# Kernel optimization log

Hardware: AMD Instinct MI355X
Metric: run time of the kernel (lower is better)

The kernel has to match this reference:

```python
import jax, jax.numpy as jnp
import numpy as np

B, DIN, DOUT, K = 2048, 2048, 2048, 16

def setup_inputs() -> dict:
    key = jax.random.key(0)
    k1, k2, k3 = jax.random.split(key, 3)
    # init scale from reset_parameters: s = 3**0.5 / ((din+dout)/2 * k)**0.25
    d = (DIN + DOUT) / 2.0
    s = 3.0 ** 0.5 / (d * K) ** 0.25
    x = jax.random.normal(k1, (B, DIN), dtype=jnp.float32)
    w1 = jax.random.uniform(k2, (DIN, DOUT, K), minval=-s, maxval=s, dtype=jnp.float32)
    w2 = jax.random.uniform(k3, (DIN, DOUT, K), minval=-s, maxval=s, dtype=jnp.float32)
    b1 = jnp.zeros((DOUT, K), dtype=jnp.float32)
    b2 = jnp.zeros((DOUT,), dtype=jnp.float32)
    return {"x": x, "w1": w1, "b1": b1, "w2": w2, "b2": b2}

def reference(x, w1, b1, w2, b2):
    # g: [b, o, k] gating mixture, relu-activated
    g = jax.nn.relu(jnp.einsum('bi,iok->bok', x, w1) + b1)
    # three-way contraction over i and k -> [b, o]
    out = jnp.einsum('bi,iok,bok->bo', x, w2, g) + b2
    return out
```

## Files before the change

kernel.cpp:

```cpp
#include <hip/hip_runtime.h>
#include <hip/hip_bf16.h>


typedef __bf16 bf16;
typedef bf16 bf16x8 __attribute__((ext_vector_type(8)));
typedef bf16 bf16x4 __attribute__((ext_vector_type(4)));
typedef float f32x4 __attribute__((ext_vector_type(4)));

typedef __attribute__((address_space(1))) const void gco_void;
typedef __attribute__((address_space(3))) void lds_void;

#define DIN_   2048
#define DOUT_  2048
#define NP_    32768

__device__ __forceinline__ bf16x8 cvt8(f32x4 a, f32x4 b) {
    bf16x8 v;
    v[0] = (bf16)a[0]; v[1] = (bf16)a[1]; v[2] = (bf16)a[2]; v[3] = (bf16)a[3];
    v[4] = (bf16)b[0]; v[5] = (bf16)b[1]; v[6] = (bf16)b[2]; v[7] = (bf16)b[3];
    return v;
}

__global__ __launch_bounds__(256)
void xcvt(const float* __restrict__ x, bf16* __restrict__ xb) {
    const size_t i = ((size_t)blockIdx.x * 256 + threadIdx.x) * 8;
    f32x4 a = *(const f32x4*)(x + i);
    f32x4 b = *(const f32x4*)(x + i + 4);
    *(bf16x8*)(xb + i) = cvt8(a, b);
}

__global__ __launch_bounds__(256)
void wtrans(const float* __restrict__ w1, const float* __restrict__ w2,
            bf16* __restrict__ w1t, bf16* __restrict__ w2t) {
    __shared__ float s[64][65];
    const int t  = threadIdx.x;
    const int lr = t >> 4;
    const int lq = t & 15;
    const int n0 = blockIdx.x * 64;
    const int i0 = blockIdx.y * 64;
    const float* src = blockIdx.z ? w2 : w1;
    bf16*        dst = blockIdx.z ? w2t : w1t;
#pragma unroll
    for (int r = 0; r < 4; ++r) {
        const int il = lr + 16 * r;
        f32x4 v = *(const f32x4*)(src + (size_t)(i0 + il) * NP_ + n0 + lq * 4);
        s[il][lq * 4 + 0] = v[0]; s[il][lq * 4 + 1] = v[1];
        s[il][lq * 4 + 2] = v[2]; s[il][lq * 4 + 3] = v[3];
    }
    __syncthreads();
#pragma unroll
    for (int r = 0; r < 4; ++r) {
        const int nl = lr + 16 * r;
        bf16x4 o;
        o[0] = (bf16)s[lq * 4 + 0][nl]; o[1] = (bf16)s[lq * 4 + 1][nl];
        o[2] = (bf16)s[lq * 4 + 2][nl]; o[3] = (bf16)s[lq * 4 + 3][nl];
        *(bf16x4*)(dst + (size_t)(n0 + nl) * DIN_ + i0 + lq * 4) = o;
    }
}

#define SYNC8() do { asm volatile("s_waitcnt vmcnt(8)" ::: "memory"); \
    __builtin_amdgcn_s_barrier(); __builtin_amdgcn_sched_barrier(0); } while (0)
#define SYNC4() do { asm volatile("s_waitcnt vmcnt(4)" ::: "memory"); \
    __builtin_amdgcn_s_barrier(); __builtin_amdgcn_sched_barrier(0); } while (0)
#define SYNC0() do { asm volatile("s_waitcnt vmcnt(0)" ::: "memory"); \
    __builtin_amdgcn_s_barrier(); __builtin_amdgcn_sched_barrier(0); } while (0)

__global__ __launch_bounds__(512, 2)
void mix2_gemmr(const bf16* __restrict__ xb, const bf16* __restrict__ w1t,
                const bf16* __restrict__ w2t, const float* __restrict__ b1,
                const float* __restrict__ b2, float* __restrict__ out)
{
    __shared__ alignas(16) char lds[131072];

    const int tid  = threadIdx.x;
    const int lane = tid & 63;
    const int wid  = tid >> 6;
    const int wm   = wid >> 2;
    const int wn   = wid & 3;
    const int lk   = lane & 15;
    const int lg   = lane >> 4;

    const int nwg = gridDim.x;
    const int bid = (blockIdx.x & 7) * (nwg >> 3) + (blockIdx.x >> 3);
    const int mt  = bid & 7;
    const int nt  = bid >> 3;

    const int srow = tid >> 2;
    const int sswz = ((tid & 3) ^ ((srow >> 1) & 3)) * 8;
    const bf16* gA  = xb  + (size_t)(mt * 256 + srow) * DIN_ + sswz;
    const bf16* gB1 = w1t + (size_t)(nt * 128 + srow) * DIN_ + sswz;
    const bf16* gB2 = w2t + (size_t)(nt * 128 + srow) * DIN_ + sswz;

    const int kswz = (lg ^ ((lk >> 1) & 3)) * 16;
    int aoff[8], boff[2];
#pragma unroll
    for (int fm = 0; fm < 8; ++fm) aoff[fm] = (wm * 128 + fm * 16 + lk) * 64 + kswz;
#pragma unroll
    for (int fn = 0; fn < 2; ++fn) boff[fn] = (wn * 32 + fn * 16 + lk) * 64 + kswz;

    f32x4 acc1[8][2], acc2[8][2];
#pragma unroll
    for (int i = 0; i < 8; ++i)
#pragma unroll
        for (int j = 0; j < 2; ++j) {
            acc1[i][j] = (f32x4){0.f, 0.f, 0.f, 0.f};
            acc2[i][j] = (f32x4){0.f, 0.f, 0.f, 0.f};
        }

    const int ldw = wid * 1024;
    auto STG = [&](int h) {
        char* r = lds + (h & 3) * 32768;
        const int koff = h * 32;
        __builtin_amdgcn_global_load_lds((gco_void*)(gA  + koff),             (lds_void*)(r +         ldw), 16, 0, 0);
        __builtin_amdgcn_global_load_lds((gco_void*)(gA + 128 * DIN_ + koff), (lds_void*)(r +  8192 + ldw), 16, 0, 0);
        __builtin_amdgcn_global_load_lds((gco_void*)(gB1 + koff),             (lds_void*)(r + 16384 + ldw), 16, 0, 0);
        __builtin_amdgcn_global_load_lds((gco_void*)(gB2 + koff),             (lds_void*)(r + 24576 + ldw), 16, 0, 0);
    };

    auto PHASE = [&](int h) {
        const char* r = lds + (h & 3) * 32768;
        bf16x8 a[8], u[2], v[2];
#pragma unroll
        for (int fn = 0; fn < 2; ++fn) {
            u[fn] = *(const bf16x8*)(r + 16384 + boff[fn]);
            v[fn] = *(const bf16x8*)(r + 24576 + boff[fn]);
        }
#pragma unroll
        for (int fm = 0; fm < 8; ++fm) a[fm] = *(const bf16x8*)(r + aoff[fm]);
        __builtin_amdgcn_s_setprio(1);
#pragma unroll
        for (int fm = 0; fm < 8; ++fm)
#pragma unroll
            for (int fn = 0; fn < 2; ++fn) {
                acc1[fm][fn] = __builtin_amdgcn_mfma_f32_16x16x32_bf16(a[fm], u[fn], acc1[fm][fn], 0, 0, 0);
                acc2[fm][fn] = __builtin_amdgcn_mfma_f32_16x16x32_bf16(a[fm], v[fn], acc2[fm][fn], 0, 0, 0);
            }
        __builtin_amdgcn_s_setprio(0);
    };

    STG(0); STG(1); STG(2);

#pragma unroll 1
    for (int t = 0; t < 15; ++t) {
        const int h0 = t * 4;
#pragma unroll
        for (int q = 0; q < 4; ++q) {
            SYNC8();
            STG(h0 + q + 3);
            PHASE(h0 + q);
        }
    }
    SYNC8(); STG(63); PHASE(60);
    SYNC8();          PHASE(61);
    SYNC4();          PHASE(62);
    SYNC0();          PHASE(63);

    const int obase = nt * 8 + wn * 2;
#pragma unroll
    for (int fn = 0; fn < 2; ++fn) {
        const int o = obase + fn;
        const float bb1 = b1[(size_t)o * 16 + lk];
        const float bb2 = b2[o];
#pragma unroll
        for (int fm = 0; fm < 8; ++fm) {
#pragma unroll
            for (int j = 0; j < 4; ++j) {
                float g = fmaxf(acc1[fm][fn][j] + bb1, 0.f);
                float p = g * acc2[fm][fn][j];
                p += __shfl_xor(p, 1);
                p += __shfl_xor(p, 2);
                p += __shfl_xor(p, 4);
                p += __shfl_xor(p, 8);
                if (lk == 0) {
                    const int brow = mt * 256 + wm * 128 + fm * 16 + lg * 4 + j;
                    out[(size_t)brow * DOUT_ + o] = p + bb2;
                }
            }
        }
    }
}

__global__ __launch_bounds__(512)
void mix2_fused_direct(const float* __restrict__ x, const float* __restrict__ w1,
                       const float* __restrict__ b1, const float* __restrict__ w2,
                       const float* __restrict__ b2, float* __restrict__ out)
{
    __shared__ alignas(16) char lds[2 * 49152];

    const int tid  = threadIdx.x;
    const int lane = tid & 63;
    const int wid  = tid >> 6;
    const int wm   = wid >> 2;
    const int wn   = wid & 3;

    const int nwg = gridDim.x;
    const int bid = (blockIdx.x & 7) * (nwg >> 3) + (blockIdx.x >> 3);
    const int mt  = bid & 15;
    const int nt  = bid >> 4;

    const int lk  = lane & 15;
    const int lg  = lane >> 4;
    const int swz = (lane & 7) << 4;

    const int a_row  = tid >> 3;
    const int a_col8 = tid & 7;
    const int b_ib = ((tid >> 5) & 15) << 2;
    const int b_nb = (tid & 31) << 2;

    const float* pa  = x  + (size_t)(mt * 128 + a_row) * DIN_ + a_col8 * 8;
    const float* pb1 = w1 + (size_t)b_ib * NP_ + (size_t)nt * 128 + b_nb;
    const float* pb2 = w2 + (size_t)b_ib * NP_ + (size_t)nt * 128 + b_nb;

    const int aswz   = (a_col8 * 16) ^ ((a_row & 7) << 4);
    const int aoffw0 = a_row * 128 + aswz;
    const int aoffw1 = (a_row + 64) * 128 + aswz;

    int aoff[4], boff1[2], boff2[2];
#pragma unroll
    for (int fm = 0; fm < 4; ++fm) aoff[fm] = (wm * 64 + fm * 16 + lk) * 128;
#pragma unroll
    for (int fn = 0; fn < 2; ++fn) {
        const int n = wn * 32 + fn * 16 + lk;
        boff1[fn] = 16384 + n * 128;
        boff2[fn] = 32768 + n * 128;
    }
    const int kp0 = (lg * 16) ^ swz;
    const int kp1 = (64 + lg * 16) ^ swz;

    f32x4 acc1[4][2], acc2[4][2];
#pragma unroll
    for (int i = 0; i < 4; ++i)
#pragma unroll
        for (int j = 0; j < 2; ++j) {
            acc1[i][j] = (f32x4){0.f, 0.f, 0.f, 0.f};
            acc2[i][j] = (f32x4){0.f, 0.f, 0.f, 0.f};
        }

    f32x4 rA[4], rB1[4], rB2[4];

    auto LOAD = [&](int kt) {
        const float* a0 = pa + kt * 64;
        rA[0] = *(const f32x4*)(a0);
        rA[1] = *(const f32x4*)(a0 + 4);
        rA[2] = *(const f32x4*)(a0 + (size_t)64 * DIN_);
        rA[3] = *(const f32x4*)(a0 + (size_t)64 * DIN_ + 4);
        const float* q1 = pb1 + (size_t)kt * 64 * NP_;
        const float* q2 = pb2 + (size_t)kt * 64 * NP_;
#pragma unroll
        for (int j = 0; j < 4; ++j) {
            rB1[j] = *(const f32x4*)(q1 + (size_t)j * NP_);
            rB2[j] = *(const f32x4*)(q2 + (size_t)j * NP_);
        }
    };

    auto STORE = [&](char* s) {
        *(bf16x8*)(s + aoffw0) = cvt8(rA[0], rA[1]);
        *(bf16x8*)(s + aoffw1) = cvt8(rA[2], rA[3]);
        char* s1 = s + 16384;
        char* s2 = s + 32768;
#pragma unroll
        for (int c = 0; c < 4; ++c) {
            const int n   = b_nb + c;
            const int off = n * 128 + ((b_ib * 2) ^ ((n & 7) << 4));
            bf16x4 v1, v2;
            v1[0] = (bf16)rB1[0][c]; v1[1] = (bf16)rB1[1][c];
            v1[2] = (bf16)rB1[2][c]; v1[3] = (bf16)rB1[3][c];
            v2[0] = (bf16)rB2[0][c]; v2[1] = (bf16)rB2[1][c];
            v2[2] = (bf16)rB2[2][c]; v2[3] = (bf16)rB2[3][c];
            *(bf16x4*)(s1 + off) = v1;
            *(bf16x4*)(s2 + off) = v2;
        }
    };

    auto COMPUTE = [&](const char* s) {
#pragma unroll
        for (int kb = 0; kb < 2; ++kb) {
            const int kp = kb ? kp1 : kp0;
            bf16x8 a[4], u[2], v[2];
#pragma unroll
            for (int fm = 0; fm < 4; ++fm) a[fm] = *(const bf16x8*)(s + aoff[fm] + kp);
#pragma unroll
            for (int fn = 0; fn < 2; ++fn) u[fn] = *(const bf16x8*)(s + boff1[fn] + kp);
#pragma unroll
            for (int fn = 0; fn < 2; ++fn) v[fn] = *(const bf16x8*)(s + boff2[fn] + kp);
#pragma unroll
            for (int fm = 0; fm < 4; ++fm)
#pragma unroll
                for (int fn = 0; fn < 2; ++fn) {
                    acc1[fm][fn] = __builtin_amdgcn_mfma_f32_16x16x32_bf16(a[fm], u[fn], acc1[fm][fn], 0, 0, 0);
                    acc2[fm][fn] = __builtin_amdgcn_mfma_f32_16x16x32_bf16(a[fm], v[fn], acc2[fm][fn], 0, 0, 0);
                }
        }
    };

    char* buf0 = lds;
    char* buf1 = lds + 49152;

    LOAD(0);
    STORE(buf0);
    __syncthreads();

    for (int kt = 0; kt < 32; ++kt) {
        if (kt + 1 < 32) LOAD(kt + 1);
        COMPUTE((kt & 1) ? buf1 : buf0);
        if (kt + 1 < 32) {
            STORE((kt & 1) ? buf0 : buf1);
            __syncthreads();
        }
    }

    const int obase = nt * 8 + wn * 2;
#pragma unroll
    for (int fn = 0; fn < 2; ++fn) {
        const int o = obase + fn;
        const float bb1 = b1[(size_t)o * 16 + lk];
        const float bb2 = b2[o];
#pragma unroll
        for (int fm = 0; fm < 4; ++fm) {
#pragma unroll
            for (int j = 0; j < 4; ++j) {
                float g = fmaxf(acc1[fm][fn][j] + bb1, 0.f);
                float p = g * acc2[fm][fn][j];
                p += __shfl_xor(p, 1);
                p += __shfl_xor(p, 2);
                p += __shfl_xor(p, 4);
                p += __shfl_xor(p, 8);
                if (lk == 0) {
                    const int brow = mt * 128 + wm * 64 + fm * 16 + lg * 4 + j;
                    out[(size_t)brow * DOUT_ + o] = p + bb2;
                }
            }
        }
    }
}

extern "C" void kernel_launch(void* const* d_in, const int* in_sizes, int n_in,
                              void* d_out, int out_size, void* d_ws, size_t ws_size,
                              hipStream_t stream) {
    (void)in_sizes; (void)n_in; (void)out_size;
    const float* x  = (const float*)d_in[0];
    const float* w1 = (const float*)d_in[1];
    const float* b1 = (const float*)d_in[2];
    const float* w2 = (const float*)d_in[3];
    const float* b2 = (const float*)d_in[4];
    float* out = (float*)d_out;

    const size_t XB   = (size_t)DIN_ * DIN_ * 2;
    const size_t WT   = (size_t)NP_ * DIN_ * 2;
    const size_t NEED = XB + 2 * WT;

    if (ws_size >= NEED) {
        bf16* xb  = (bf16*)d_ws;
        bf16* w1t = (bf16*)((char*)d_ws + XB);
        bf16* w2t = (bf16*)((char*)d_ws + XB + WT);
        hipLaunchKernelGGL(xcvt,   dim3(2048),       dim3(256), 0, stream, x, xb);
        hipLaunchKernelGGL(wtrans, dim3(512, 32, 2), dim3(256), 0, stream, w1, w2, w1t, w2t);
        hipLaunchKernelGGL(mix2_gemmr, dim3(2048),   dim3(512), 0, stream, xb, w1t, w2t, b1, b2, out);
    } else {
        hipLaunchKernelGGL(mix2_fused_direct, dim3(4096), dim3(512), 0, stream, x, w1, b1, w2, b2, out);
    }
}
```

Baseline: 683.1 us.

## Split each K-step into two ping-pong halves interleaving loads and MFMA

Restructures the main GEMM loop so each K-step runs as two halves. Each half reads part of the A fragments from LDS, issues half of the next stage's global-to-LDS loads, then runs a block of MFMAs between barriers. This is the 8-wave ping-pong pattern, meant to overlap LDS reads and global loads with matrix work across the two co-resident workgroups. It adds more barriers per step, and the vmcnt waits in the tail must still match the pipeline depth for correctness.

```diff
diff --git a/kernel.cpp b/kernel.cpp
--- a/kernel.cpp
+++ b/kernel.cpp
@@ -58,17 +58,10 @@
     }
 }
 
-#define SYNC8() do { asm volatile("s_waitcnt vmcnt(8)" ::: "memory"); \
-    __builtin_amdgcn_s_barrier(); __builtin_amdgcn_sched_barrier(0); } while (0)
-#define SYNC4() do { asm volatile("s_waitcnt vmcnt(4)" ::: "memory"); \
-    __builtin_amdgcn_s_barrier(); __builtin_amdgcn_sched_barrier(0); } while (0)
-#define SYNC0() do { asm volatile("s_waitcnt vmcnt(0)" ::: "memory"); \
-    __builtin_amdgcn_s_barrier(); __builtin_amdgcn_sched_barrier(0); } while (0)
-
 __global__ __launch_bounds__(512, 2)
-void mix2_gemmr(const bf16* __restrict__ xb, const bf16* __restrict__ w1t,
-                const bf16* __restrict__ w2t, const float* __restrict__ b1,
-                const float* __restrict__ b2, float* __restrict__ out)
+void mix2_gemm8p(const bf16* __restrict__ xb, const bf16* __restrict__ w1t,
+                 const bf16* __restrict__ w2t, const float* __restrict__ b1,
+                 const float* __restrict__ b2, float* __restrict__ out)
 {
     __shared__ alignas(16) char lds[131072];
 
@@ -108,52 +101,78 @@
         }
 
     const int ldw = wid * 1024;
-    auto STG = [&](int h) {
+    auto STG_A = [&](int h) {
         char* r = lds + (h & 3) * 32768;
         const int koff = h * 32;
-        __builtin_amdgcn_global_load_lds((gco_void*)(gA  + koff),             (lds_void*)(r +         ldw), 16, 0, 0);
-        __builtin_amdgcn_global_load_lds((gco_void*)(gA + 128 * DIN_ + koff), (lds_void*)(r +  8192 + ldw), 16, 0, 0);
-        __builtin_amdgcn_global_load_lds((gco_void*)(gB1 + koff),             (lds_void*)(r + 16384 + ldw), 16, 0, 0);
-        __builtin_amdgcn_global_load_lds((gco_void*)(gB2 + koff),             (lds_void*)(r + 24576 + ldw), 16, 0, 0);
-    };
-
-    auto PHASE = [&](int h) {
-        const char* r = lds + (h & 3) * 32768;
-        bf16x8 a[8], u[2], v[2];
-#pragma unroll
-        for (int fn = 0; fn < 2; ++fn) {
-            u[fn] = *(const bf16x8*)(r + 16384 + boff[fn]);
-            v[fn] = *(const bf16x8*)(r + 24576 + boff[fn]);
-        }
-#pragma unroll
-        for (int fm = 0; fm < 8; ++fm) a[fm] = *(const bf16x8*)(r + aoff[fm]);
-        __builtin_amdgcn_s_setprio(1);
-#pragma unroll
-        for (int fm = 0; fm < 8; ++fm)
-#pragma unroll
-            for (int fn = 0; fn < 2; ++fn) {
-                acc1[fm][fn] = __builtin_amdgcn_mfma_f32_16x16x32_bf16(a[fm], u[fn], acc1[fm][fn], 0, 0, 0);
-                acc2[fm][fn] = __builtin_amdgcn_mfma_f32_16x16x32_bf16(a[fm], v[fn], acc2[fm][fn], 0, 0, 0);
-            }
-        __builtin_amdgcn_s_setprio(0);
-    };
-
-    STG(0); STG(1); STG(2);
+        __builtin_amdgcn_global_load_lds((gco_void*)(gA  + koff),             (lds_void*)(r +        ldw), 16, 0, 0);
+        __builtin_amdgcn_global_load_lds((gco_void*)(gA + 128 * DIN_ + koff), (lds_void*)(r + 8192 + ldw), 16, 0, 0);
+    };
+    auto STG_B = [&](int h) {
+        char* r = lds + (h & 3) * 32768;
+        const int koff = h * 32;
+        __builtin_amdgcn_global_load_lds((gco_void*)(gB1 + koff), (lds_void*)(r + 16384 + ldw), 16, 0, 0);
+        __builtin_amdgcn_global_load_lds((gco_void*)(gB2 + koff), (lds_void*)(r + 24576 + ldw), 16, 0, 0);
+    };
+
+#define HALF(h, DO_STG, W) do {                                              \
+    const char* r_ = lds + (((h) & 3) * 32768);                              \
+    bf16x8 u[2], v[2], a0[4], a1[4];                                         \
+                                                      \
+    _Pragma("unroll") for (int fn_ = 0; fn_ < 2; ++fn_) {                    \
+        u[fn_] = *(const bf16x8*)(r_ + 16384 + boff[fn_]);                   \
+        v[fn_] = *(const bf16x8*)(r_ + 24576 + boff[fn_]);                   \
+    }                                                                        \
+    _Pragma("unroll") for (int j_ = 0; j_ < 4; ++j_)                         \
+        a0[j_] = *(const bf16x8*)(r_ + aoff[j_]);                            \
+    if (DO_STG) STG_A((h) + 3);                                              \
+    __builtin_amdgcn_s_barrier();                                            \
+    asm volatile("s_waitcnt lgkmcnt(0)" ::: "memory");                       \
+    __builtin_amdgcn_sched_barrier(0);                                       \
+    __builtin_amdgcn_s_setprio(1);                                           \
+    _Pragma("unroll") for (int j_ = 0; j_ < 4; ++j_)                         \
+        _Pragma("unroll") for (int fn_ = 0; fn_ < 2; ++fn_) {                \
+            acc1[j_][fn_] = __builtin_amdgcn_mfma_f32_16x16x32_bf16(a0[j_], u[fn_], acc1[j_][fn_], 0, 0, 0); \
+            acc2[j_][fn_] = __builtin_amdgcn_mfma_f32_16x16x32_bf16(a0[j_], v[fn_], acc2[j_][fn_], 0, 0, 0); \
+        }                                                                    \
+    __builtin_amdgcn_s_setprio(0);                                           \
+    __builtin_amdgcn_s_barrier();                                            \
+                                                      \
+    _Pragma("unroll") for (int j_ = 0; j_ < 4; ++j_)                         \
+        a1[j_] = *(const bf16x8*)(r_ + aoff[4 + j_]);                        \
+    if (DO_STG) STG_B((h) + 3);                                              \
+    __builtin_amdgcn_s_barrier();                                            \
+    asm volatile("s_waitcnt lgkmcnt(0)" ::: "memory");                       \
+    __builtin_amdgcn_sched_barrier(0);                                       \
+    __builtin_amdgcn_s_setprio(1);                                           \
+    _Pragma("unroll") for (int j_ = 0; j_ < 4; ++j_)                         \
+        _Pragma("unroll") for (int fn_ = 0; fn_ < 2; ++fn_) {                \
+            acc1[4 + j_][fn_] = __builtin_amdgcn_mfma_f32_16x16x32_bf16(a1[j_], u[fn_], acc1[4 + j_][fn_], 0, 0, 0); \
+            acc2[4 + j_][fn_] = __builtin_amdgcn_mfma_f32_16x16x32_bf16(a1[j_], v[fn_], acc2[4 + j_][fn_], 0, 0, 0); \
+        }                                                                    \
+    __builtin_amdgcn_s_setprio(0);                                           \
+    asm volatile("s_waitcnt vmcnt(" #W ")" ::: "memory");                    \
+    __builtin_amdgcn_s_barrier();                                            \
+} while (0)
+
+    STG_A(0); STG_B(0); STG_A(1); STG_B(1); STG_A(2); STG_B(2);
+    asm volatile("s_waitcnt vmcnt(8)" ::: "memory");
+    __builtin_amdgcn_s_barrier();
+    __builtin_amdgcn_sched_barrier(0);
 
 #pragma unroll 1
     for (int t = 0; t < 15; ++t) {
         const int h0 = t * 4;
-#pragma unroll
-        for (int q = 0; q < 4; ++q) {
-            SYNC8();
-            STG(h0 + q + 3);
-            PHASE(h0 + q);
-        }
-    }
-    SYNC8(); STG(63); PHASE(60);
-    SYNC8();          PHASE(61);
-    SYNC4();          PHASE(62);
-    SYNC0();          PHASE(63);
+        HALF(h0 + 0, true, 8);
+        HALF(h0 + 1, true, 8);
+        HALF(h0 + 2, true, 8);
+        HALF(h0 + 3, true, 8);
+    }
+    HALF(60, true, 8);
+    HALF(61, false, 4);
+    HALF(62, false, 0);
+    HALF(63, false, 0);
+
+#undef HALF
 
     const int obase = nt * 8 + wn * 2;
 #pragma unroll
@@ -355,7 +374,7 @@
         bf16* w2t = (bf16*)((char*)d_ws + XB + WT);
         hipLaunchKernelGGL(xcvt,   dim3(2048),       dim3(256), 0, stream, x, xb);
         hipLaunchKernelGGL(wtrans, dim3(512, 32, 2), dim3(256), 0, stream, w1, w2, w1t, w2t);
-        hipLaunchKernelGGL(mix2_gemmr, dim3(2048),   dim3(512), 0, stream, xb, w1t, w2t, b1, b2, out);
+        hipLaunchKernelGGL(mix2_gemm8p, dim3(2048),  dim3(512), 0, stream, xb, w1t, w2t, b1, b2, out);
     } else {
         hipLaunchKernelGGL(mix2_fused_direct, dim3(4096), dim3(512), 0, stream, x, w1, b1, w2, b2, out);
     }
```

New measurement: 680.1 us. No clear change (-0.4%).

## Split GEMM workgroup into 16 waves with halved per-wave M tile

Applied to the files above, without the earlier changes.

Grows the main GEMM workgroup from 512 to 1024 threads (16 waves) on the same 256x128 output tile. Each wave now covers 64 rows instead of 128, which halves its accumulators and A-fragment registers. Global-to-LDS staging is redistributed so each thread issues two loads per stage instead of four, and the vmcnt waits are adjusted to match. The aim is more waves per CU for latency hiding, since the launch bound goes from (512,2) to (1024,1). The cost is the same LDS use per block with more waves contending at each barrier, and every B fragment is now re-read from LDS by twice as many waves.

```diff
diff --git a/kernel.cpp b/kernel.cpp
--- a/kernel.cpp
+++ b/kernel.cpp
@@ -58,17 +58,10 @@
     }
 }
 
-#define SYNC8() do { asm volatile("s_waitcnt vmcnt(8)" ::: "memory"); \
-    __builtin_amdgcn_s_barrier(); __builtin_amdgcn_sched_barrier(0); } while (0)
-#define SYNC4() do { asm volatile("s_waitcnt vmcnt(4)" ::: "memory"); \
-    __builtin_amdgcn_s_barrier(); __builtin_amdgcn_sched_barrier(0); } while (0)
-#define SYNC0() do { asm volatile("s_waitcnt vmcnt(0)" ::: "memory"); \
-    __builtin_amdgcn_s_barrier(); __builtin_amdgcn_sched_barrier(0); } while (0)
-
-__global__ __launch_bounds__(512, 2)
-void mix2_gemmr(const bf16* __restrict__ xb, const bf16* __restrict__ w1t,
-                const bf16* __restrict__ w2t, const float* __restrict__ b1,
-                const float* __restrict__ b2, float* __restrict__ out)
+__global__ __launch_bounds__(1024, 1)
+void mix2_gemm16w(const bf16* __restrict__ xb, const bf16* __restrict__ w1t,
+                  const bf16* __restrict__ w2t, const float* __restrict__ b1,
+                  const float* __restrict__ b2, float* __restrict__ out)
 {
     __shared__ alignas(16) char lds[131072];
 
@@ -85,51 +78,52 @@
     const int mt  = bid & 7;
     const int nt  = bid >> 3;
 
-    const int srow = tid >> 2;
-    const int sswz = ((tid & 3) ^ ((srow >> 1) & 3)) * 8;
-    const bf16* gA  = xb  + (size_t)(mt * 256 + srow) * DIN_ + sswz;
-    const bf16* gB1 = w1t + (size_t)(nt * 128 + srow) * DIN_ + sswz;
-    const bf16* gB2 = w2t + (size_t)(nt * 128 + srow) * DIN_ + sswz;
+    const int arow = tid >> 2;
+    const int aswz = ((tid & 3) ^ ((arow >> 1) & 3)) * 8;
+    const int tb   = tid & 511;
+    const int brow = tb >> 2;
+    const int bswz = ((tb & 3) ^ ((brow >> 1) & 3)) * 8;
+    const bf16* gA = xb + (size_t)(mt * 256 + arow) * DIN_ + aswz;
+    const bf16* gB = (tid < 512 ? w1t : w2t) + (size_t)(nt * 128 + brow) * DIN_ + bswz;
+    const int adst = arow * 64 + (tid & 3) * 16;
+    const int bdst = 16384 + (tid >= 512 ? 8192 : 0) + tb * 16;
 
     const int kswz = (lg ^ ((lk >> 1) & 3)) * 16;
-    int aoff[8], boff[2];
-#pragma unroll
-    for (int fm = 0; fm < 8; ++fm) aoff[fm] = (wm * 128 + fm * 16 + lk) * 64 + kswz;
-#pragma unroll
-    for (int fn = 0; fn < 2; ++fn) boff[fn] = (wn * 32 + fn * 16 + lk) * 64 + kswz;
-
-    f32x4 acc1[8][2], acc2[8][2];
-#pragma unroll
-    for (int i = 0; i < 8; ++i)
+    int aoff[4], boff[2];
+#pragma unroll
+    for (int fm = 0; fm < 4; ++fm) aoff[fm] = (wm * 64 + fm * 16 + lk) * 64 + kswz;
+#pragma unroll
+    for (int fn = 0; fn < 2; ++fn) boff[fn] = 16384 + (wn * 32 + fn * 16 + lk) * 64 + kswz;
+
+    f32x4 acc1[4][2], acc2[4][2];
+#pragma unroll
+    for (int i = 0; i < 4; ++i)
 #pragma unroll
         for (int j = 0; j < 2; ++j) {
             acc1[i][j] = (f32x4){0.f, 0.f, 0.f, 0.f};
             acc2[i][j] = (f32x4){0.f, 0.f, 0.f, 0.f};
         }
 
-    const int ldw = wid * 1024;
     auto STG = [&](int h) {
         char* r = lds + (h & 3) * 32768;
         const int koff = h * 32;
-        __builtin_amdgcn_global_load_lds((gco_void*)(gA  + koff),             (lds_void*)(r +         ldw), 16, 0, 0);
-        __builtin_amdgcn_global_load_lds((gco_void*)(gA + 128 * DIN_ + koff), (lds_void*)(r +  8192 + ldw), 16, 0, 0);
-        __builtin_amdgcn_global_load_lds((gco_void*)(gB1 + koff),             (lds_void*)(r + 16384 + ldw), 16, 0, 0);
-        __builtin_amdgcn_global_load_lds((gco_void*)(gB2 + koff),             (lds_void*)(r + 24576 + ldw), 16, 0, 0);
+        __builtin_amdgcn_global_load_lds((gco_void*)(gA + koff), (lds_void*)(r + adst), 16, 0, 0);
+        __builtin_amdgcn_global_load_lds((gco_void*)(gB + koff), (lds_void*)(r + bdst), 16, 0, 0);
     };
 
     auto PHASE = [&](int h) {
         const char* r = lds + (h & 3) * 32768;
-        bf16x8 a[8], u[2], v[2];
+        bf16x8 a[4], u[2], v[2];
 #pragma unroll
         for (int fn = 0; fn < 2; ++fn) {
-            u[fn] = *(const bf16x8*)(r + 16384 + boff[fn]);
-            v[fn] = *(const bf16x8*)(r + 24576 + boff[fn]);
-        }
-#pragma unroll
-        for (int fm = 0; fm < 8; ++fm) a[fm] = *(const bf16x8*)(r + aoff[fm]);
+            u[fn] = *(const bf16x8*)(r + boff[fn]);
+            v[fn] = *(const bf16x8*)(r + boff[fn] + 8192);
+        }
+#pragma unroll
+        for (int fm = 0; fm < 4; ++fm) a[fm] = *(const bf16x8*)(r + aoff[fm]);
         __builtin_amdgcn_s_setprio(1);
 #pragma unroll
-        for (int fm = 0; fm < 8; ++fm)
+        for (int fm = 0; fm < 4; ++fm)
 #pragma unroll
             for (int fn = 0; fn < 2; ++fn) {
                 acc1[fm][fn] = __builtin_amdgcn_mfma_f32_16x16x32_bf16(a[fm], u[fn], acc1[fm][fn], 0, 0, 0);
@@ -138,6 +132,9 @@
         __builtin_amdgcn_s_setprio(0);
     };
 
+#define SYNC(W) do { asm volatile("s_waitcnt vmcnt(" #W ")" ::: "memory"); \
+    __builtin_amdgcn_s_barrier(); __builtin_amdgcn_sched_barrier(0); } while (0)
+
     STG(0); STG(1); STG(2);
 
 #pragma unroll 1
@@ -145,15 +142,17 @@
         const int h0 = t * 4;
 #pragma unroll
         for (int q = 0; q < 4; ++q) {
-            SYNC8();
+            SYNC(4);
             STG(h0 + q + 3);
             PHASE(h0 + q);
         }
     }
-    SYNC8(); STG(63); PHASE(60);
-    SYNC8();          PHASE(61);
-    SYNC4();          PHASE(62);
-    SYNC0();          PHASE(63);
+    SYNC(4); STG(63); PHASE(60);
+    SYNC(4);          PHASE(61);
+    SYNC(2);          PHASE(62);
+    SYNC(0);          PHASE(63);
+
+#undef SYNC
 
     const int obase = nt * 8 + wn * 2;
 #pragma unroll
@@ -162,7 +161,7 @@
         const float bb1 = b1[(size_t)o * 16 + lk];
         const float bb2 = b2[o];
 #pragma unroll
-        for (int fm = 0; fm < 8; ++fm) {
+        for (int fm = 0; fm < 4; ++fm) {
 #pragma unroll
             for (int j = 0; j < 4; ++j) {
                 float g = fmaxf(acc1[fm][fn][j] + bb1, 0.f);
@@ -172,8 +171,8 @@
                 p += __shfl_xor(p, 4);
                 p += __shfl_xor(p, 8);
                 if (lk == 0) {
-                    const int brow = mt * 256 + wm * 128 + fm * 16 + lg * 4 + j;
-                    out[(size_t)brow * DOUT_ + o] = p + bb2;
+                    const int brow2 = mt * 256 + wm * 64 + fm * 16 + lg * 4 + j;
+                    out[(size_t)brow2 * DOUT_ + o] = p + bb2;
                 }
             }
         }
@@ -353,9 +352,9 @@
         bf16* xb  = (bf16*)d_ws;
         bf16* w1t = (bf16*)((char*)d_ws + XB);
         bf16* w2t = (bf16*)((char*)d_ws + XB + WT);
-        hipLaunchKernelGGL(xcvt,   dim3(2048),       dim3(256), 0, stream, x, xb);
-        hipLaunchKernelGGL(wtrans, dim3(512, 32, 2), dim3(256), 0, stream, w1, w2, w1t, w2t);
-        hipLaunchKernelGGL(mix2_gemmr, dim3(2048),   dim3(512), 0, stream, xb, w1t, w2t, b1, b2, out);
+        hipLaunchKernelGGL(xcvt,   dim3(2048),        dim3(256),  0, stream, x, xb);
+        hipLaunchKernelGGL(wtrans, dim3(512, 32, 2),  dim3(256),  0, stream, w1, w2, w1t, w2t);
+        hipLaunchKernelGGL(mix2_gemm16w, dim3(2048),  dim3(1024), 0, stream, xb, w1t, w2t, b1, b2, out);
     } else {
         hipLaunchKernelGGL(mix2_fused_direct, dim3(4096), dim3(512), 0, stream, x, w1, b1, w2, b2, out);
     }
```

Result: faster. 642.8 us (-5.9%).
